# Kernel optimization log

Measured on AMD Instinct MI355X. Metric: run time of the kernel, lower is better.

The kernel has to match this reference:

```python
import jax, jax.numpy as jnp
import numpy as np
import math

B, S, E, H, DFF = 8, 1024, 1024, 16, 4096
HD = E // H
EPS = 1e-05


def setup_inputs() -> dict:
    key = jax.random.key(0)
    ks = jax.random.split(key, 8)
    wb_attn = math.sqrt(3.0 / E)
    wb1 = math.sqrt(3.0 * 2.0 / E)      # kaiming for linear1 (in=E)
    wb2 = math.sqrt(3.0 * 2.0 / DFF)    # kaiming for linear2 (in=DFF)
    return {
        "x": jax.random.normal(ks[0], (B, S, E), jnp.float32),
        "in_weights": jax.random.uniform(ks[1], (3, E, E), jnp.float32, -wb_attn, wb_attn),
        "out_weights": jax.random.uniform(ks[2], (E, E), jnp.float32, -wb_attn, wb_attn),
        "ln1_scale": jnp.ones((E,), jnp.float32),
        "ln1_bias": jnp.zeros((E,), jnp.float32),
        "ln2_scale": jnp.ones((E,), jnp.float32),
        "ln2_bias": jnp.zeros((E,), jnp.float32),
        "w1": jax.random.uniform(ks[3], (DFF, E), jnp.float32, -wb1, wb1),
        "b1": jnp.zeros((DFF,), jnp.float32),
        "w2": jax.random.uniform(ks[4], (E, DFF), jnp.float32, -wb2, wb2),
        "b2": jnp.zeros((E,), jnp.float32),
    }


def _layernorm(x, scale, bias):
    mean = jnp.mean(x, axis=-1, keepdims=True)
    var = jnp.var(x, axis=-1, keepdims=True, ddof=1)  # torch.var unbiased=True
    return scale * (x - mean) / jnp.sqrt(var + EPS) + bias


def reference(x, in_weights, out_weights, ln1_scale, ln1_bias, ln2_scale, ln2_bias, w1, b1, w2, b2):
    # QKV projections: note key uses in_weights[0], query [1], value [2]
    def proj(w):  # (B,S,E) -> (B,H,S,HD)
        return (x @ w).reshape(B, S, H, HD).transpose(0, 2, 1, 3)
    k = proj(in_weights[0])
    q = proj(in_weights[1])
    v = proj(in_weights[2])
    scores = jnp.einsum("bhsd,bhtd->bhst", q, k) / math.sqrt(HD)
    probs = jax.nn.softmax(scores, axis=-1)
    attn = jnp.einsum("bhst,bhtd->bhsd", probs, v).transpose(0, 2, 1, 3).reshape(B, S, E)
    attn_out = attn @ out_weights
    # quirk preserved: residual is attn_out + dropout(attn_out) = 2*attn_out (eval mode)
    x1 = _layernorm(attn_out + attn_out, ln1_scale, ln1_bias)
    ffn = jax.nn.relu(x1 @ w1.T + b1) @ w2.T + b2
    return _layernorm(x1 + ffn, ln2_scale, ln2_bias)
```

## Files before the change

### kernel.cpp

```cpp
#include <hip/hip_runtime.h>

#define E_DIM 1024
#define S_LEN 1024
#define H_NUM 16
#define HD_DIM 64
#define B_NUM 8
#define DFF_DIM 4096
#define NROWS 8192
#define QKV_LD 3072

typedef unsigned short u16;
typedef unsigned u32;
typedef short bf16v8 __attribute__((ext_vector_type(8)));
typedef float f32x4 __attribute__((ext_vector_type(4)));
typedef float f32x16 __attribute__((ext_vector_type(16)));

#define QK_SCALE 0.18033688011112042f

__device__ __forceinline__ u16 f2b(float f) {
  union { float f; unsigned u; } x; x.f = f;
  return (u16)((x.u + 0x7fffu + ((x.u >> 16) & 1u)) >> 16);
}

__device__ __forceinline__ void gload16(const void* g, void* l) {
  __builtin_amdgcn_global_load_lds((const __attribute__((address_space(1))) void*)g,
                                   (__attribute__((address_space(3))) void*)l, 16, 0, 0);
}

template<int MODE>
__global__ __launch_bounds__(512, 2) void gemm8(
    const u16* __restrict__ A, const u16* __restrict__ Bt,
    void* __restrict__ C0, void* __restrict__ C1, const float* __restrict__ bias,
    int N, int KA, int nxt, int NT) {
  __shared__ u16 sA[2 * 16384];
  __shared__ u16 sB[2 * 16384];

  const int tid = threadIdx.x;
  const int lane = tid & 63;
  const int wid = tid >> 6;
  const int wm = wid >> 2, wn = wid & 3;
  const int l15 = lane & 15, l4 = lane >> 4;
  const int pk0 = l4 ^ (l15 & 7);

  const int gx = gridDim.x;
  const int lin = blockIdx.y * gx + blockIdx.x;
  const int chunk = (gx * gridDim.y) >> 3;
  const int swz = (lin & 7) * chunk + (lin >> 3);
  const int bym = swz / gx, bxm = swz % gx;
  const int kh = (bxm >= nxt) ? 1 : 0;
  const int bm = bym * 256;
  const int bn = (bxm - kh * nxt) * 256;
  const int k0 = kh * NT * 64;

  const int srow = tid >> 3;
  const int gch = ((tid & 7) ^ (srow & 7)) * 8;
  const u16* Ag[4];
  const u16* Bg[4];
#pragma unroll
  for (int i = 0; i < 4; ++i) {
    Ag[i] = A + k0 + (size_t)(bm + i * 64 + srow) * KA + gch;
    Bg[i] = Bt + k0 + (size_t)(bn + i * 64 + srow) * KA + gch;
  }
  const int t8 = tid * 8;

#define ST1(tile, li)                                                              \
  do {                                                                             \
    if ((li) < 4) gload16(Ag[li] + (tile) * 64, sA + ((tile)&1) * 16384 + (li)*4096 + t8); \
    else gload16(Bg[(li)-4] + (tile) * 64, sB + ((tile)&1) * 16384 + ((li)-4) * 4096 + t8); \
  } while (0)
#define STG8(tile)                                         \
  if ((tile) < NT) {                                       \
    _Pragma("unroll") for (int li = 0; li < 8; ++li) ST1(tile, li); \
  }

  bf16v8 a[4][2], b[4][2];
  f32x4 acc[8][4];
#pragma unroll
  for (int m = 0; m < 8; ++m)
#pragma unroll
    for (int n = 0; n < 4; ++n) acc[m][n] = (f32x4){0.f, 0.f, 0.f, 0.f};

#define LDA(mh, buf)                                                        \
  {                                                                         \
    _Pragma("unroll") for (int mp = 0; mp < 4; ++mp) {                      \
      const u16* rp = (buf) + (size_t)(wm * 128 + (mh)*64 + mp * 16 + l15) * 64; \
      a[mp][0] = *(const bf16v8*)(rp + pk0 * 8);                            \
      a[mp][1] = *(const bf16v8*)(rp + (pk0 ^ 4) * 8);                      \
    }                                                                       \
  }
#define LDB(n0, buf)                                                        \
  {                                                                         \
    _Pragma("unroll") for (int nn = (n0); nn < (n0) + 2; ++nn) {            \
      const u16* rp = (buf) + (size_t)(wn * 64 + nn * 16 + l15) * 64;       \
      b[nn][0] = *(const bf16v8*)(rp + pk0 * 8);                            \
      b[nn][1] = *(const bf16v8*)(rp + (pk0 ^ 4) * 8);                      \
    }                                                                       \
  }
#define MMPH(mh, n0)                                                                      \
  {                                                                                       \
    __builtin_amdgcn_s_setprio(1);                                                        \
    _Pragma("unroll") for (int mp = 0; mp < 4; ++mp) {                                    \
      _Pragma("unroll") for (int nn = (n0); nn < (n0) + 2; ++nn) {                        \
        acc[(mh)*4 + mp][nn] = __builtin_amdgcn_mfma_f32_16x16x32_bf16(                   \
            a[mp][0], b[nn][0], acc[(mh)*4 + mp][nn], 0, 0, 0);                           \
        acc[(mh)*4 + mp][nn] = __builtin_amdgcn_mfma_f32_16x16x32_bf16(                   \
            a[mp][1], b[nn][1], acc[(mh)*4 + mp][nn], 0, 0, 0);                           \
      }                                                                                   \
    }                                                                                     \
    __builtin_amdgcn_s_setprio(0);                                                        \
  }

  STG8(0);
  STG8(1);
  __builtin_amdgcn_sched_barrier(0);
  asm volatile("s_waitcnt vmcnt(8)" ::: "memory");
  __builtin_amdgcn_s_barrier();
  LDA(0, sA);
  LDB(0, sB);

  for (int t = 0; t < NT; ++t) {
    u16* sAc = sA + (t & 1) * 16384;
    u16* sBc = sB + (t & 1) * 16384;
    u16* sAn = sA + ((t + 1) & 1) * 16384;
    u16* sBn = sB + ((t + 1) & 1) * 16384;
    MMPH(0, 0);
    LDB(2, sBc);
    __builtin_amdgcn_s_barrier();
    MMPH(0, 2);
    LDA(1, sAc);
    __builtin_amdgcn_s_barrier();
    STG8(t + 2);
    MMPH(1, 0);
    __builtin_amdgcn_sched_barrier(0);
    if (t + 2 < NT)      asm volatile("s_waitcnt vmcnt(8)" ::: "memory");
    else if (t + 1 < NT) asm volatile("s_waitcnt vmcnt(0)" ::: "memory");
    __builtin_amdgcn_s_barrier();
    MMPH(1, 2);
    if (t + 1 < NT) {
      LDA(0, sAn);
      LDB(0, sBn);
    }
    __builtin_amdgcn_s_barrier();
  }

  const int lrow0 = bm + wm * 128 + l4 * 4;
  const int lcol0 = bn + wn * 64 + l15;
  const float scl = (MODE == 0 && ((bn >> 10) == 1)) ? QK_SCALE : 1.f;
  void* Cw = kh ? C1 : C0;
#pragma unroll
  for (int m = 0; m < 8; ++m) {
#pragma unroll
    for (int n = 0; n < 4; ++n) {
      const int col = lcol0 + n * 16;
      float bv = 0.f;
      if (MODE == 2) bv = bias[col];
      if (MODE == 3) bv = kh ? 0.f : bias[col];
#pragma unroll
      for (int i = 0; i < 4; ++i) {
        const int row = lrow0 + m * 16 + i;
        float v = acc[m][n][i] + bv;
        if (MODE == 2) v = fmaxf(v, 0.f);
        if (MODE == 0) v *= scl;
        if (MODE == 0 || MODE == 2)
          ((u16*)Cw)[(size_t)row * N + col] = f2b(v);
        else
          ((float*)Cw)[(size_t)row * N + col] = v;
      }
    }
  }
#undef ST1
#undef STG8
#undef LDA
#undef LDB
#undef MMPH
}

#define MKPF(dst, A0, B0, C0, D0)                                             \
  {                                                                           \
    u32 sa = (u32)__shfl_xor((int)(A0), 32), sb = (u32)__shfl_xor((int)(B0), 32); \
    u32 sc = (u32)__shfl_xor((int)(C0), 32), sd = (u32)__shfl_xor((int)(D0), 32); \
    union { u32 u[4]; bf16v8 v; } cc;                                         \
    cc.u[0] = hi ? sc : (A0); cc.u[1] = hi ? sd : (B0);                       \
    cc.u[2] = hi ? (C0) : sa; cc.u[3] = hi ? (D0) : sb;                       \
    dst = cc.v;                                                               \
  }

__device__ __forceinline__ void vt_write64(u16* sVtBuf, int4 wv, int vr, int s8) {
  int4 w2;
  w2.x = __shfl_xor(wv.x, 8); w2.y = __shfl_xor(wv.y, 8);
  w2.z = __shfl_xor(wv.z, 8); w2.w = __shfl_xor(wv.w, 8);
  const int t = vr >> 1;
  const int odd = vr & 1;
  const u16* own = (const u16*)&wv;
  const u16* par = (const u16*)&w2;
  char* dstbase = (char*)sVtBuf + (t >> 2) * 1024 + (t & 3) * 4;
#pragma unroll
  for (int k = 0; k < 4; k++) {
    const unsigned lo = odd ? (unsigned)par[4 + k] : (unsigned)own[k];
    const unsigned h2 = odd ? (unsigned)own[4 + k] : (unsigned)par[k];
    const int d = s8 * 8 + k + (odd ? 4 : 0);
    const int dsw = d ^ s8;
    *(unsigned*)(dstbase + dsw * 16) = lo | (h2 << 16);
  }
}

__global__ __launch_bounds__(512, 4) void attn_fa(
    const u16* __restrict__ qkv, u16* __restrict__ attn) {
  __shared__ u16 sK[2][64 * 64];
  __shared__ u16 sVt[2][64 * 64];

  const int tid = threadIdx.x, lane = tid & 63;
  const int l31 = lane & 31, hi = lane >> 5;
  const int w = ((blockIdx.x & 7) << 6) + (blockIdx.x >> 3);
  const int bh = w >> 2;
  const int b = bh >> 4, h = bh & 15;
  const int qrow0 = (w & 3) * 256 + (tid >> 6) * 32;
  const size_t rowb = (size_t)b * S_LEN * QKV_LD;
  const u16* kg = qkv + rowb + h * HD_DIM;
  const u16* qg = qkv + rowb + 1024 + h * HD_DIM;
  const u16* vg = qkv + rowb + 2048 + h * HD_DIM;
  const size_t obase = (size_t)b * (S_LEN * E_DIM) + (size_t)h * HD_DIM;

  bf16v8 qf[4];
#pragma unroll
  for (int ks = 0; ks < 4; ++ks)
    qf[ks] = *(const bf16v8*)(qg + (size_t)(qrow0 + l31) * QKV_LD + ks * 16 + hi * 8);

  const int kr = tid >> 3;
  const int s8 = tid & 7;
  const u16* kgsrc = kg + (size_t)kr * QKV_LD + ((s8 ^ (kr & 7)) * 8);
  const u16* vgsrc = vg + (size_t)kr * QKV_LD + s8 * 8;

  f32x16 accT[2];
#pragma unroll
  for (int i = 0; i < 16; ++i) { accT[0][i] = 0.f; accT[1][i] = 0.f; }
  float mrun = -1e30f, lrun = 0.f;

  gload16(kgsrc, sK[0] + tid * 8);
  {
    int4 v0 = *(const int4*)(vgsrc);
    vt_write64(sVt[0], v0, kr, s8);
  }
  __syncthreads();

  for (int t = 0; t < 16; ++t) {
    const int cur = t & 1;
    int4 vreg;
    if (t < 15) {
      gload16(kgsrc + (size_t)(t + 1) * 64 * QKV_LD, sK[cur ^ 1] + tid * 8);
      vreg = *(const int4*)(vgsrc + (size_t)(t + 1) * 64 * QKV_LD);
    }

    f32x16 T0, T1;
#pragma unroll
    for (int i = 0; i < 16; ++i) { T0[i] = 0.f; T1[i] = 0.f; }
#pragma unroll
    for (int ks = 0; ks < 4; ++ks) {
      const int ch = ((2 * ks + hi) ^ (l31 & 7)) * 8;
      const bf16v8 k0 = *(const bf16v8*)(sK[cur] + (size_t)l31 * 64 + ch);
      const bf16v8 k1 = *(const bf16v8*)(sK[cur] + (size_t)(32 + l31) * 64 + ch);
      T0 = __builtin_amdgcn_mfma_f32_32x32x16_bf16(k0, qf[ks], T0, 0, 0, 0);
      T1 = __builtin_amdgcn_mfma_f32_32x32x16_bf16(k1, qf[ks], T1, 0, 0, 0);
    }

    float mx = fmaxf(T0[0], T1[0]);
#pragma unroll
    for (int r = 1; r < 16; ++r) mx = fmaxf(mx, fmaxf(T0[r], T1[r]));
    mx = fmaxf(mx, __shfl_xor(mx, 32));
    const bool skip = __all(mx <= mrun + 8.f);
    const float mnew = skip ? mrun : fmaxf(mrun, mx);
    float rs = 0.f;
#pragma unroll
    for (int r = 0; r < 16; ++r) { T0[r] = exp2f(T0[r] - mnew); rs += T0[r]; }
#pragma unroll
    for (int r = 0; r < 16; ++r) { T1[r] = exp2f(T1[r] - mnew); rs += T1[r]; }
    rs += __shfl_xor(rs, 32);
    if (skip) {
      lrun += rs;
    } else {
      const float esc = exp2f(mrun - mnew);
      mrun = mnew;
      lrun = lrun * esc + rs;
#pragma unroll
      for (int r = 0; r < 16; ++r) { accT[0][r] *= esc; accT[1][r] *= esc; }
    }

    u32 P0[8], P1[8];
#pragma unroll
    for (int wd = 0; wd < 8; ++wd) {
      asm("v_cvt_pk_bf16_f32 %0, %1, %2" : "=v"(P0[wd]) : "v"(T0[2 * wd]), "v"(T0[2 * wd + 1]));
      asm("v_cvt_pk_bf16_f32 %0, %1, %2" : "=v"(P1[wd]) : "v"(T1[2 * wd]), "v"(T1[2 * wd + 1]));
    }
    bf16v8 pf[4];
    MKPF(pf[0], P0[0], P0[1], P0[2], P0[3]);
    MKPF(pf[1], P0[4], P0[5], P0[6], P0[7]);
    MKPF(pf[2], P1[0], P1[1], P1[2], P1[3]);
    MKPF(pf[3], P1[4], P1[5], P1[6], P1[7]);

#pragma unroll
    for (int dblk = 0; dblk < 2; ++dblk) {
      const int dd = dblk * 32 + l31;
      const int drow = (dd ^ (dd >> 3)) * 8;
#pragma unroll
      for (int ks = 0; ks < 4; ++ks) {
        const bf16v8 va = *(const bf16v8*)(sVt[cur] + (2 * ks + hi) * 512 + drow);
        accT[dblk] = __builtin_amdgcn_mfma_f32_32x32x16_bf16(va, pf[ks], accT[dblk], 0, 0, 0);
      }
    }

    if (t < 15) vt_write64(sVt[cur ^ 1], vreg, kr, s8);
    __syncthreads();
  }

  const float linv = 1.f / lrun;
  u16* orow = attn + obase + (size_t)(qrow0 + l31) * E_DIM;
#pragma unroll
  for (int dblk = 0; dblk < 2; ++dblk)
#pragma unroll
    for (int a4 = 0; a4 < 4; ++a4) {
      ushort4 st;
      st.x = f2b(accT[dblk][4 * a4 + 0] * linv);
      st.y = f2b(accT[dblk][4 * a4 + 1] * linv);
      st.z = f2b(accT[dblk][4 * a4 + 2] * linv);
      st.w = f2b(accT[dblk][4 * a4 + 3] * linv);
      *(ushort4*)(orow + dblk * 32 + a4 * 8 + hi * 4) = st;
    }
}

template<int MODE>
__global__ __launch_bounds__(256) void ln_kernel(
    const float* __restrict__ a, const float* __restrict__ b2nd, const float* __restrict__ c3rd,
    const float* __restrict__ scale, const float* __restrict__ bias,
    float* __restrict__ outf, u16* __restrict__ outb) {
  const int row = blockIdx.x;
  const int tid = threadIdx.x;
  const size_t off = (size_t)row * 1024 + tid * 4;
  float4 v = *(const float4*)(a + off);
  float4 u = *(const float4*)(b2nd + off);
  if (MODE == 0) {
    v.x = 2.f * (v.x + u.x); v.y = 2.f * (v.y + u.y);
    v.z = 2.f * (v.z + u.z); v.w = 2.f * (v.w + u.w);
  } else {
    float4 w = *(const float4*)(c3rd + off);
    v.x += u.x + w.x; v.y += u.y + w.y; v.z += u.z + w.z; v.w += u.w + w.w;
  }
  float s = v.x + v.y + v.z + v.w;
  float q = v.x * v.x + v.y * v.y + v.z * v.z + v.w * v.w;
#pragma unroll
  for (int o = 1; o < 64; o <<= 1) { s += __shfl_xor(s, o); q += __shfl_xor(q, o); }
  __shared__ float red[8];
  const int wave = tid >> 6, lane = tid & 63;
  if (lane == 0) { red[wave] = s; red[4 + wave] = q; }
  __syncthreads();
  s = red[0] + red[1] + red[2] + red[3];
  q = red[4] + red[5] + red[6] + red[7];
  const float mean = s * (1.f / 1024.f);
  const float var = (q - 1024.f * mean * mean) * (1.f / 1023.f);
  const float rstd = rsqrtf(var + 1e-5f);
  const int c = tid * 4;
  float4 sc = *(const float4*)(scale + c);
  float4 bi = *(const float4*)(bias + c);
  float4 o;
  o.x = sc.x * (v.x - mean) * rstd + bi.x;
  o.y = sc.y * (v.y - mean) * rstd + bi.y;
  o.z = sc.z * (v.z - mean) * rstd + bi.z;
  o.w = sc.w * (v.w - mean) * rstd + bi.w;
  *(float4*)(outf + off) = o;
  if (outb != nullptr) {
    ushort4 ob;
    ob.x = f2b(o.x); ob.y = f2b(o.y); ob.z = f2b(o.z); ob.w = f2b(o.w);
    *(ushort4*)(outb + off) = ob;
  }
}

__global__ __launch_bounds__(256) void cast_bf16_k(const float* __restrict__ in,
                                                   u16* __restrict__ out, int n4) {
  const int i = blockIdx.x * blockDim.x + threadIdx.x;
  if (i >= n4) return;
  float4 v = *(const float4*)(in + (size_t)i * 4);
  ushort4 o;
  o.x = f2b(v.x); o.y = f2b(v.y); o.z = f2b(v.z); o.w = f2b(v.w);
  *(ushort4*)(out + (size_t)i * 4) = o;
}

__global__ __launch_bounds__(256) void transpose_cast_k(const float* __restrict__ in,
                                                        u16* __restrict__ out) {
  __shared__ float tile[32][33];
  const int tx = threadIdx.x & 31, ty = threadIdx.x >> 5;
  const int bx = blockIdx.x * 32, by = blockIdx.y * 32;
#pragma unroll
  for (int j = 0; j < 4; j++)
    tile[ty + j * 8][tx] = in[(size_t)(by + ty + j * 8) * 1024 + bx + tx];
  __syncthreads();
#pragma unroll
  for (int j = 0; j < 4; j++)
    out[(size_t)(bx + ty + j * 8) * 1024 + by + tx] = f2b(tile[tx][ty + j * 8]);
}

extern "C" void kernel_launch(void* const* d_in, const int* in_sizes, int n_in,
                              void* d_out, int out_size, void* d_ws, size_t ws_size,
                              hipStream_t stream) {
  const float* x    = (const float*)d_in[0];
  const float* in_w = (const float*)d_in[1];
  const float* out_w = (const float*)d_in[2];
  const float* ln1s = (const float*)d_in[3];
  const float* ln1b = (const float*)d_in[4];
  const float* ln2s = (const float*)d_in[5];
  const float* ln2b = (const float*)d_in[6];
  const float* w1   = (const float*)d_in[7];
  const float* b1   = (const float*)d_in[8];
  const float* w2   = (const float*)d_in[9];
  const float* b2   = (const float*)d_in[10];
  float* outp = (float*)d_out;

  char* ws = (char*)d_ws;
  u16*   xb    = (u16*)(ws + 0);
  u16*   qkv   = (u16*)(ws + 16777216);
  u16*   attnb = (u16*)(ws + 0);
  float* attno0 = (float*)(ws + 67108864);
  float* attno1 = (float*)(ws + 100663296);
  float* x1f   = (float*)(ws + 67108864);
  u16*   x1b   = (u16*)(ws + 134217728);
  u16*   Hb    = (u16*)(ws + 0);
  float* ffn0  = (float*)(ws + 100663296);
  u16*   wkt   = (u16*)(ws + 150994944);
  u16*   wot   = wkt + 3145728;
  u16*   w1b   = wot + 1048576;
  u16*   w2b   = w1b + 4194304;
  (void)ws_size; (void)in_sizes; (void)n_in; (void)out_size;

  cast_bf16_k<<<8192, 256, 0, stream>>>(x, xb, 2097152);
  cast_bf16_k<<<4096, 256, 0, stream>>>(w1, w1b, 1048576);
  cast_bf16_k<<<4096, 256, 0, stream>>>(w2, w2b, 1048576);
  dim3 tg(32, 32);
  transpose_cast_k<<<tg, 256, 0, stream>>>(in_w + 0,       wkt);
  transpose_cast_k<<<tg, 256, 0, stream>>>(in_w + 1048576, wkt + 1048576);
  transpose_cast_k<<<tg, 256, 0, stream>>>(in_w + 2097152, wkt + 2097152);
  transpose_cast_k<<<tg, 256, 0, stream>>>(out_w,          wot);

  gemm8<0><<<dim3(12, 32), 512, 0, stream>>>(xb, wkt, qkv, nullptr, nullptr, 3072, 1024, 12, 16);

  attn_fa<<<512, 512, 0, stream>>>(qkv, attnb);

  gemm8<1><<<dim3(8, 32), 512, 0, stream>>>(attnb, wot, attno0, attno1, nullptr, 1024, 1024, 4, 8);

  ln_kernel<0><<<8192, 256, 0, stream>>>(attno0, attno1, nullptr, ln1s, ln1b, x1f, x1b);

  gemm8<2><<<dim3(16, 32), 512, 0, stream>>>(x1b, w1b, Hb, nullptr, b1, 4096, 1024, 16, 16);

  gemm8<3><<<dim3(8, 32), 512, 0, stream>>>(Hb, w2b, ffn0, outp, b2, 1024, 4096, 4, 32);

  ln_kernel<1><<<8192, 256, 0, stream>>>(x1f, ffn0, outp, ln2s, ln2b, outp, nullptr);
}
```

Before: 368.8 us.

## Store GEMM split-K partials in bf16 and read bf16 residual in layernorms

The out-projection and FFN2 split-K GEMMs now write their two partial results as bf16 instead of fp32. Both layernorm kernels read bf16 inputs, and the second layernorm takes its residual from the bf16 x1 rather than an fp32 copy, so the fp32 x1 buffer is gone. This roughly halves the memory traffic of the epilogues and layernorms. The attention kernel also uses three-input max reductions and moves the cross-half row-sum shuffle out of the loop to the end. In exchange, the partial sums and the residual lose precision before the final layernorm.

Measured after the change: 346.9 us. 1.06x faster.

```diff
diff --git a/kernel.cpp b/kernel.cpp
--- a/kernel.cpp
+++ b/kernel.cpp
@@ -20,6 +20,14 @@
 __device__ __forceinline__ u16 f2b(float f) {
   union { float f; unsigned u; } x; x.f = f;
   return (u16)((x.u + 0x7fffu + ((x.u >> 16) & 1u)) >> 16);
+}
+
+__device__ __forceinline__ float b2f(u16 v) {
+  union { unsigned u; float f; } x; x.u = ((unsigned)v) << 16; return x.f;
+}
+
+__device__ __forceinline__ float max3f(float a, float b, float c) {
+  return fmaxf(fmaxf(a, b), c);
 }
 
 __device__ __forceinline__ void gload16(const void* g, void* l) {
@@ -146,7 +154,7 @@
   const int lrow0 = bm + wm * 128 + l4 * 4;
   const int lcol0 = bn + wn * 64 + l15;
   const float scl = (MODE == 0 && ((bn >> 10) == 1)) ? QK_SCALE : 1.f;
-  void* Cw = kh ? C1 : C0;
+  u16* Cw = (u16*)(kh ? C1 : C0);
 #pragma unroll
   for (int m = 0; m < 8; ++m) {
 #pragma unroll
@@ -161,10 +169,7 @@
         float v = acc[m][n][i] + bv;
         if (MODE == 2) v = fmaxf(v, 0.f);
         if (MODE == 0) v *= scl;
-        if (MODE == 0 || MODE == 2)
-          ((u16*)Cw)[(size_t)row * N + col] = f2b(v);
-        else
-          ((float*)Cw)[(size_t)row * N + col] = v;
+        Cw[(size_t)row * N + col] = f2b(v);
       }
     }
   }
@@ -263,9 +268,13 @@
       T1 = __builtin_amdgcn_mfma_f32_32x32x16_bf16(k1, qf[ks], T1, 0, 0, 0);
     }
 
-    float mx = fmaxf(T0[0], T1[0]);
-#pragma unroll
-    for (int r = 1; r < 16; ++r) mx = fmaxf(mx, fmaxf(T0[r], T1[r]));
+    float ma = fmaxf(T0[0], T0[1]);
+#pragma unroll
+    for (int r = 2; r < 16; r += 2) ma = max3f(ma, T0[r], T0[r + 1]);
+    float mb = fmaxf(T1[0], T1[1]);
+#pragma unroll
+    for (int r = 2; r < 16; r += 2) mb = max3f(mb, T1[r], T1[r + 1]);
+    float mx = fmaxf(ma, mb);
     mx = fmaxf(mx, __shfl_xor(mx, 32));
     const bool skip = __all(mx <= mrun + 8.f);
     const float mnew = skip ? mrun : fmaxf(mrun, mx);
@@ -274,7 +283,6 @@
     for (int r = 0; r < 16; ++r) { T0[r] = exp2f(T0[r] - mnew); rs += T0[r]; }
 #pragma unroll
     for (int r = 0; r < 16; ++r) { T1[r] = exp2f(T1[r] - mnew); rs += T1[r]; }
-    rs += __shfl_xor(rs, 32);
     if (skip) {
       lrun += rs;
     } else {
@@ -312,6 +320,7 @@
     __syncthreads();
   }
 
+  lrun += __shfl_xor(lrun, 32);
   const float linv = 1.f / lrun;
   u16* orow = attn + obase + (size_t)(qrow0 + l31) * E_DIM;
 #pragma unroll
@@ -328,21 +337,25 @@
 }
 
 template<int MODE>
-__global__ __launch_bounds__(256) void ln_kernel(
-    const float* __restrict__ a, const float* __restrict__ b2nd, const float* __restrict__ c3rd,
+__global__ __launch_bounds__(256) void ln_b16(
+    const u16* __restrict__ a, const u16* __restrict__ b, const u16* __restrict__ c,
     const float* __restrict__ scale, const float* __restrict__ bias,
     float* __restrict__ outf, u16* __restrict__ outb) {
   const int row = blockIdx.x;
   const int tid = threadIdx.x;
   const size_t off = (size_t)row * 1024 + tid * 4;
-  float4 v = *(const float4*)(a + off);
-  float4 u = *(const float4*)(b2nd + off);
+  ushort4 av = *(const ushort4*)(a + off);
+  ushort4 bv = *(const ushort4*)(b + off);
+  float4 v;
+  v.x = b2f(av.x) + b2f(bv.x);
+  v.y = b2f(av.y) + b2f(bv.y);
+  v.z = b2f(av.z) + b2f(bv.z);
+  v.w = b2f(av.w) + b2f(bv.w);
   if (MODE == 0) {
-    v.x = 2.f * (v.x + u.x); v.y = 2.f * (v.y + u.y);
-    v.z = 2.f * (v.z + u.z); v.w = 2.f * (v.w + u.w);
+    v.x *= 2.f; v.y *= 2.f; v.z *= 2.f; v.w *= 2.f;
   } else {
-    float4 w = *(const float4*)(c3rd + off);
-    v.x += u.x + w.x; v.y += u.y + w.y; v.z += u.z + w.z; v.w += u.w + w.w;
+    ushort4 cv = *(const ushort4*)(c + off);
+    v.x += b2f(cv.x); v.y += b2f(cv.y); v.z += b2f(cv.z); v.w += b2f(cv.w);
   }
   float s = v.x + v.y + v.z + v.w;
   float q = v.x * v.x + v.y * v.y + v.z * v.z + v.w * v.w;
@@ -357,19 +370,20 @@
   const float mean = s * (1.f / 1024.f);
   const float var = (q - 1024.f * mean * mean) * (1.f / 1023.f);
   const float rstd = rsqrtf(var + 1e-5f);
-  const int c = tid * 4;
-  float4 sc = *(const float4*)(scale + c);
-  float4 bi = *(const float4*)(bias + c);
+  const int cc = tid * 4;
+  float4 sc = *(const float4*)(scale + cc);
+  float4 bi = *(const float4*)(bias + cc);
   float4 o;
   o.x = sc.x * (v.x - mean) * rstd + bi.x;
   o.y = sc.y * (v.y - mean) * rstd + bi.y;
   o.z = sc.z * (v.z - mean) * rstd + bi.z;
   o.w = sc.w * (v.w - mean) * rstd + bi.w;
-  *(float4*)(outf + off) = o;
-  if (outb != nullptr) {
+  if (MODE == 0) {
     ushort4 ob;
     ob.x = f2b(o.x); ob.y = f2b(o.y); ob.z = f2b(o.z); ob.w = f2b(o.w);
     *(ushort4*)(outb + off) = ob;
+  } else {
+    *(float4*)(outf + off) = o;
   }
 }
 
@@ -417,12 +431,12 @@
   u16*   xb    = (u16*)(ws + 0);
   u16*   qkv   = (u16*)(ws + 16777216);
   u16*   attnb = (u16*)(ws + 0);
-  float* attno0 = (float*)(ws + 67108864);
-  float* attno1 = (float*)(ws + 100663296);
-  float* x1f   = (float*)(ws + 67108864);
-  u16*   x1b   = (u16*)(ws + 134217728);
+  u16*   wo0   = (u16*)(ws + 67108864);
+  u16*   wo1   = (u16*)(ws + 83886080);
+  u16*   x1b   = (u16*)(ws + 100663296);
   u16*   Hb    = (u16*)(ws + 0);
-  float* ffn0  = (float*)(ws + 100663296);
+  u16*   ffn0b = (u16*)(ws + 67108864);
+  u16*   ffn1b = (u16*)(ws + 83886080);
   u16*   wkt   = (u16*)(ws + 150994944);
   u16*   wot   = wkt + 3145728;
   u16*   w1b   = wot + 1048576;
@@ -442,13 +456,13 @@
 
   attn_fa<<<512, 512, 0, stream>>>(qkv, attnb);
 
-  gemm8<1><<<dim3(8, 32), 512, 0, stream>>>(attnb, wot, attno0, attno1, nullptr, 1024, 1024, 4, 8);
-
-  ln_kernel<0><<<8192, 256, 0, stream>>>(attno0, attno1, nullptr, ln1s, ln1b, x1f, x1b);
+  gemm8<1><<<dim3(8, 32), 512, 0, stream>>>(attnb, wot, wo0, wo1, nullptr, 1024, 1024, 4, 8);
+
+  ln_b16<0><<<8192, 256, 0, stream>>>(wo0, wo1, nullptr, ln1s, ln1b, nullptr, x1b);
 
   gemm8<2><<<dim3(16, 32), 512, 0, stream>>>(x1b, w1b, Hb, nullptr, b1, 4096, 1024, 16, 16);
 
-  gemm8<3><<<dim3(8, 32), 512, 0, stream>>>(Hb, w2b, ffn0, outp, b2, 1024, 4096, 4, 32);
-
-  ln_kernel<1><<<8192, 256, 0, stream>>>(x1f, ffn0, outp, ln2s, ln2b, outp, nullptr);
-}
+  gemm8<3><<<dim3(8, 32), 512, 0, stream>>>(Hb, w2b, ffn0b, ffn1b, b2, 1024, 4096, 4, 32);
+
+  ln_b16<1><<<8192, 256, 0, stream>>>(x1b, ffn0b, ffn1b, ln2s, ln2b, outp, nullptr);
+}
```
